# Optimization experiments

Measured on AMD Instinct MI355X. Metric: run time of the kernel, lower is better.

## Reference

```python
import jax, jax.numpy as jnp
import numpy as np

T, B, L, D = 32, 128, 1024, 256  # timesteps, batch, memory slots, word_vec_size(=rnn_size)


def setup_inputs() -> dict:
    key = jax.random.key(0)
    ks = jax.random.split(key, 20)
    f = lambda k, s: jax.random.normal(k, s, dtype=jnp.float32) * 0.05
    return {
        "emb_utts": f(ks[0], (T, B, D)),
        "hr0": f(ks[1], (B, D)),
        "cr0": f(ks[2], (B, D)),
        "hw0": f(ks[3], (B, D)),
        "cw0": f(ks[4], (B, D)),
        "M": f(ks[5], (B, L, D)),
        "mask": jax.random.randint(ks[6], (B, L), 0, 2).astype(bool),
        "Wih_r": f(ks[7], (4 * D, D)),
        "Whh_r": f(ks[8], (4 * D, D)),
        "bih_r": f(ks[9], (4 * D,)),
        "bhh_r": f(ks[10], (4 * D,)),
        "Wc": f(ks[11], (D, 2 * D)),
        "bc": f(ks[12], (D,)),
        "Wih_w": f(ks[13], (4 * D, D)),
        "Whh_w": f(ks[14], (4 * D, D)),
        "bih_w": f(ks[15], (4 * D,)),
        "bhh_w": f(ks[16], (4 * D,)),
    }


def _lstm_cell(x, h, c, Wih, Whh, bih, bhh):
    # PyTorch LSTMCell gate order: i, f, g, o
    g = x @ Wih.T + h @ Whh.T + bih + bhh
    i, fg, gg, o = jnp.split(g, 4, axis=1)
    i = jax.nn.sigmoid(i)
    fg = jax.nn.sigmoid(fg)
    gg = jnp.tanh(gg)
    o = jax.nn.sigmoid(o)
    c2 = fg * c + i * gg
    return o * jnp.tanh(c2), c2


def reference(emb_utts, hr0, cr0, hw0, cw0, M, mask,
              Wih_r, Whh_r, bih_r, bhh_r, Wc, bc,
              Wih_w, Whh_w, bih_w, bhh_w):
    def step(carry, w):
        hr, cr, hw, cw, Mc = carry
        hr, cr = _lstm_cell(w, hr, cr, Wih_r, Whh_r, bih_r, bhh_r)
        # attention read: z = softmax(masked(hr . M))  -> [B, L]
        z = jnp.einsum('bd,bld->bl', hr, Mc)
        z = jax.nn.softmax(jnp.where(mask, -jnp.inf, z), axis=1)
        m = jnp.einsum('bl,bld->bd', z, Mc)           # gather read [B, D]
        comp = jax.nn.softmax(jnp.concatenate([hr, m], axis=1) @ Wc.T + bc, axis=1)
        hw, cw = _lstm_cell(comp, hw, cw, Wih_w, Whh_w, bih_w, bhh_w)
        # memory rewrite exactly as source: M_new = (1 - z) + hw * z (broadcast)
        Mc = (1.0 - z[:, :, None]) + hw[:, None, :] * z[:, :, None]
        return (hr, cr, hw, cw, Mc), hw

    (hr, cr, hw, cw, M), outputs = jax.lax.scan(
        step, (hr0, cr0, hw0, cw0, M), emb_utts)
    return outputs, hr, cr, hw, cw, M
```

## Files before the change

kernel.cpp:

```cpp
#include <hip/hip_runtime.h>
#include <math.h>

typedef unsigned int u32;
typedef __attribute__((ext_vector_type(2))) _Float16 h2;

#define kT 32
#define OUT_STATES 1048576
#define OUT_M      1179648

union H2U { u32 u; h2 h; };

__device__ __forceinline__ float dot2u(u32 w, u32 x, float acc){
  H2U a; a.u = w; H2U b; b.u = x;
#if __has_builtin(__builtin_amdgcn_fdot2)
  return __builtin_amdgcn_fdot2(a.h, b.h, acc, false);
#else
  acc += (float)a.h.x * (float)b.h.x;
  acc += (float)a.h.y * (float)b.h.y;
  return acc;
#endif
}

__device__ __forceinline__ u32 packf16(float x, float y){
  H2U v; v.h.x = (_Float16)x; v.h.y = (_Float16)y; return v.u;
}

__device__ __forceinline__ u32 alu(const u32* p){
  return __hip_atomic_load((u32*)p, __ATOMIC_RELAXED, __HIP_MEMORY_SCOPE_AGENT);
}
__device__ __forceinline__ float alf(const float* p){
  return __hip_atomic_load((float*)p, __ATOMIC_RELAXED, __HIP_MEMORY_SCOPE_AGENT);
}
__device__ __forceinline__ void asu(u32* p, u32 v){
  __hip_atomic_store(p, v, __ATOMIC_RELAXED, __HIP_MEMORY_SCOPE_AGENT);
}
__device__ __forceinline__ void asf(float* p, float v){
  __hip_atomic_store(p, v, __ATOMIC_RELAXED, __HIP_MEMORY_SCOPE_AGENT);
}

__device__ __forceinline__ void pollk(const u32* f, int n, u32 tgt, int tid){
  if (tid < 64){
    const u32* p = f + ((tid < n) ? tid : 0);
    for (;;){
      if (__all((int)(alu(p) >= tgt))) break;
      __builtin_amdgcn_s_sleep(2);
    }
  }
  __syncthreads();
}

__global__ __launch_bounds__(1024) void k_prep(
        const float* __restrict__ Wih_r, const float* __restrict__ Whh_r,
        const float* __restrict__ bih_r, const float* __restrict__ bhh_r,
        const float* __restrict__ Wc,    const float* __restrict__ bc,
        const float* __restrict__ Wih_w, const float* __restrict__ Whh_w,
        const float* __restrict__ bih_w, const float* __restrict__ bhh_w,
        const unsigned char* __restrict__ maskraw,
        u32* WAp, u32* WEp, u32* Wcp, float* bA, float* bE, float* bcf,
        float* wcs, unsigned char* mbuf, u32* flags){
  __shared__ int sb[3];
  if (threadIdx.x < 3) sb[threadIdx.x] = 0;
  __syncthreads();
  if (threadIdx.x < 512){
    unsigned char c = maskraw[threadIdx.x];
    if (c > 1u) atomicOr(&sb[0], 1);
    if ((threadIdx.x & 3) != 0 && c != 0) atomicOr(&sb[1], 1);
    if ((threadIdx.x & 3) == 1 && c == 0x3F) atomicOr(&sb[2], 1);
  }
  __syncthreads();
  int mode = (!sb[0]) ? (sb[1] ? 1 : 0) : (sb[2] ? 2 : 3);

  int idx = blockIdx.x * 1024 + threadIdx.x;
  if (idx < 262144){
    int col = idx >> 8, kp = idx & 255;
    int k0 = 2 * kp;
    float v0 = (k0 < 256) ? Wih_r[col * 256 + k0] : Whh_r[col * 256 + k0 - 256];
    float v1 = (k0 < 256) ? Wih_r[col * 256 + k0 + 1]
                          : Whh_r[col * 256 + k0 + 1 - 256];
    WAp[kp * 1024 + col] = packf16(v0, v1);
  } else if (idx < 524288){
    int i = idx - 262144;
    int col = i >> 8, kp = i & 255;
    int k0 = 2 * kp;
    float v0 = (k0 < 256) ? Wih_w[col * 256 + k0] : Whh_w[col * 256 + k0 - 256];
    float v1 = (k0 < 256) ? Wih_w[col * 256 + k0 + 1]
                          : Whh_w[col * 256 + k0 + 1 - 256];
    WEp[kp * 1024 + col] = packf16(v0, v1);
  } else if (idx < 589824){
    int i = idx - 524288;
    int col = i >> 8, kp = i & 255;
    Wcp[kp * 256 + col] = packf16(Wc[col * 512 + 2 * kp], Wc[col * 512 + 2 * kp + 1]);
  } else if (idx < 590848){
    int i = idx - 589824;
    bA[i] = bih_r[i] + bhh_r[i];
  } else if (idx < 591872){
    int i = idx - 590848;
    bE[i] = bih_w[i] + bhh_w[i];
  } else if (idx < 592128){
    int i = idx - 591872;
    bcf[i] = bc[i];
  } else if (idx < 592384){
    int c = idx - 592128;
    float s = 0.f;
    for (int k = 0; k < 256; k++) s += Wc[c * 512 + 256 + k];
    wcs[c] = s;
  } else if (idx < 723456){
    int l = idx - 592384;
    unsigned char mv;
    if      (mode == 0) mv = (((const int*)maskraw)[l] != 0);
    else if (mode == 1) mv = (maskraw[l] != 0);
    else if (mode == 2) mv = ((maskraw[2*l] | maskraw[2*l+1]) != 0);
    else                mv = (((const unsigned int*)maskraw)[l] != 0);
    mbuf[l] = mv;
  } else if (idx < 724224){
    flags[idx - 723456] = 0;
  }
}

__global__ __launch_bounds__(1024) void k_pre(
        const float* __restrict__ emb, const u32* __restrict__ WAp,
        u32* __restrict__ gxp){
  __shared__ u32 wt[16384];
  __shared__ u32 xt[128 * 129];
  int t = blockIdx.x, c0 = blockIdx.y * 128, tid = threadIdx.x;
  for (int i = 0; i < 16; i++){
    int idx = i * 1024 + tid;
    wt[idx] = WAp[(size_t)(idx >> 7) * 1024 + c0 + (idx & 127)];
    int b = idx >> 7, kp = idx & 127;
    float2 e2 = *(const float2*)(emb + (size_t)t * 32768 + b * 256 + 2 * kp);
    xt[b * 129 + kp] = packf16(e2.x, e2.y);
  }
  __syncthreads();
  int b = tid & 127, cg = tid >> 7;
  float acc[16];
  #pragma unroll
  for (int j = 0; j < 16; j++) acc[j] = 0.f;
  const u32* xrow = xt + b * 129;
  for (int kp = 0; kp < 128; kp++){
    u32 xv = xrow[kp];
    const uint4* wr = (const uint4*)(wt + kp * 128 + cg * 16);
    #pragma unroll
    for (int j4 = 0; j4 < 4; j4++){
      uint4 wv = wr[j4];
      acc[4*j4+0] = dot2u(wv.x, xv, acc[4*j4+0]);
      acc[4*j4+1] = dot2u(wv.y, xv, acc[4*j4+1]);
      acc[4*j4+2] = dot2u(wv.z, xv, acc[4*j4+2]);
      acc[4*j4+3] = dot2u(wv.w, xv, acc[4*j4+3]);
    }
  }
  u32* gp = gxp + ((size_t)t * 128 + b) * 512 + (c0 >> 1) + cg * 8;
  #pragma unroll
  for (int i = 0; i < 8; i++) gp[i] = packf16(acc[2*i], acc[2*i+1]);
}

__device__ __forceinline__ void gemv256(const u32* __restrict__ W,
        const u32* xh, float* psum, int tid){
  int cg = tid & 255, ks = tid >> 8;
  const uint4* wp = (const uint4*)W + (size_t)ks * 32 * 256 + cg;
  const u32* xk = xh + ks * 32;
  float a0 = 0.f, a1 = 0.f, a2 = 0.f, a3 = 0.f;
  #pragma unroll 8
  for (int i = 0; i < 32; i++){
    uint4 wv = wp[(size_t)i * 256];
    u32 xp = xk[i];
    a0 = dot2u(wv.x, xp, a0);  a1 = dot2u(wv.y, xp, a1);
    a2 = dot2u(wv.z, xp, a2);  a3 = dot2u(wv.w, xp, a3);
  }
  float4 r; r.x = a0; r.y = a1; r.z = a2; r.w = a3;
  *(float4*)&psum[ks * 1024 + cg * 4] = r;
}

__device__ __forceinline__ void gemv128x256(const u32* __restrict__ W,
        const u32* xh, float* psum, int tid){
  int c = tid & 255, ks = tid >> 8;
  const u32* wp = W + (size_t)(ks * 32) * 256 + c;
  const u32* xk = xh + ks * 32;
  float a = 0.f;
  #pragma unroll 8
  for (int i = 0; i < 32; i++) a = dot2u(wp[(size_t)i * 256], xk[i], a);
  psum[ks * 256 + c] = a;
}

__device__ void scan_half(int k, const float* __restrict__ M0,
        const unsigned char* __restrict__ mbuf, const float* __restrict__ hrf,
        float* spbuf, float* mpbuf, float* msbuf, u32* fT0, const u32* fR,
        char* sc, int tid){
  float* ps   = (float*)(sc);
  float* wred = (float*)(sc + 16640);
  float* sred = (float*)(sc + 16704);
  float* hr0l = (float*)(sc + 16768);
  int row = k >> 1, half = k & 1;
  pollk(fR + row, 1, 1u, tid);
  if (tid < 256) hr0l[tid] = alf(hrf + row * 256 + tid);
  __syncthreads();
  int w = tid >> 6, lane = tid & 63;
  float4 hrv = *(const float4*)&hr0l[lane * 4];
  float run_max = -INFINITY, S = 0.f;
  float m0 = 0.f, m1 = 0.f, m2 = 0.f, m3 = 0.f;
  int l0 = half * 512 + w * 32;
  for (int l = l0; l < l0 + 32; ++l){
    float4 Mv = *(const float4*)(M0 + ((size_t)row * 1024 + l) * 256 + lane * 4);
    float part = Mv.x * hrv.x + Mv.y * hrv.y + Mv.z * hrv.z + Mv.w * hrv.w;
    #pragma unroll
    for (int mm = 32; mm >= 1; mm >>= 1) part += __shfl_xor(part, mm, 64);
    float s = mbuf[row * 1024 + l] ? -INFINITY : part;
    if (lane == 0) asf(spbuf + row * 1024 + l, s);
    float nm = fmaxf(run_max, s);
    if (nm > -INFINITY){
      float sc2 = expf(run_max - nm);
      float p   = expf(s - nm);
      S = S * sc2 + p;
      m0 = m0 * sc2 + p * Mv.x;  m1 = m1 * sc2 + p * Mv.y;
      m2 = m2 * sc2 + p * Mv.z;  m3 = m3 * sc2 + p * Mv.w;
      run_max = nm;
    }
  }
  if (lane == 0){ wred[w] = run_max; sred[w] = S; }
  ps[w * 260 + lane * 4 + 0] = m0;
  ps[w * 260 + lane * 4 + 1] = m1;
  ps[w * 260 + lane * 4 + 2] = m2;
  ps[w * 260 + lane * 4 + 3] = m3;
  __syncthreads();
  float gmax = -INFINITY;
  #pragma unroll
  for (int w2 = 0; w2 < 16; w2++) gmax = fmaxf(gmax, wred[w2]);
  float Sg = 0.f;
  #pragma unroll
  for (int w2 = 0; w2 < 16; w2++) Sg += sred[w2] * expf(wred[w2] - gmax);
  if (tid < 256){
    float mv = 0.f;
    #pragma unroll
    for (int w2 = 0; w2 < 16; w2++) mv += ps[w2 * 260 + tid] * expf(wred[w2] - gmax);
    asf(mpbuf + k * 256 + tid, mv);
  }
  if (tid == 0){ asf(msbuf + 2 * k, gmax); asf(msbuf + 2 * k + 1, Sg); }
  __syncthreads();
  if (tid == 0) asu(fT0 + k, 1u);
}

__global__ __launch_bounds__(1024, 4) void k_main(
        const float* __restrict__ hr0, const float* __restrict__ cr0,
        const float* __restrict__ hw0, const float* __restrict__ cw0,
        const float* __restrict__ M0,
        const u32* __restrict__ WAp, const u32* __restrict__ WEp,
        const u32* __restrict__ Wcp, const float* __restrict__ bA,
        const float* __restrict__ bE, const float* __restrict__ bcf,
        const float* __restrict__ wcs, const unsigned char* __restrict__ mbuf,
        const u32* __restrict__ gxp,
        float* __restrict__ hrf, float* __restrict__ ubuf,
        float* __restrict__ gwbuf,
        u32* __restrict__ hwp, float* __restrict__ zsbuf,
        float* __restrict__ hwfin, float* __restrict__ spbuf,
        float* __restrict__ mpbuf, float* __restrict__ msbuf,
        u32* __restrict__ flags, float* __restrict__ out){
  __shared__ __attribute__((aligned(16))) char smem[86016];
  int bid = blockIdx.x, tid = threadIdx.x;
  int w = tid >> 6, lane = tid & 63;
  u32* fR  = flags;
  u32* fG  = flags + 192;
  u32* fW  = flags + 256;
  u32* fT0 = flags + 320;

  if (bid < 128){
    int b = bid;
    float* psum = (float*)(smem);
    u32*  xh    = (u32*)(smem + 16384);
    float* hr_f = (float*)(smem + 16896);
    const u32* WRh = WAp + 128 * 1024;
    float cst = (tid < 256) ? cr0[b * 256 + tid] : 0.f;
    if (tid < 128){
      float2 h0 = *(const float2*)(hr0 + b * 256 + 2 * tid);
      xh[tid] = packf16(h0.x, h0.y);
    }
    __syncthreads();
    for (int t = 0; t < kT; t++){
      if (t >= 2) pollk(fW + (b >> 1), 1, (u32)(t - 1), tid);
      u32 gx0 = 0, gx1 = 0, gx2 = 0, gx3 = 0;
      if (tid < 256){
        const u32* gx = gxp + ((size_t)t * 128 + b) * 512;
        gx0 = gx[tid >> 1];          gx1 = gx[128 + (tid >> 1)];
        gx2 = gx[256 + (tid >> 1)];  gx3 = gx[384 + (tid >> 1)];
      }
      gemv256(WRh, xh, psum, tid);
      __syncthreads();
      if (tid < 256){
        H2U p0, p1, p2, p3;
        p0.u = gx0; p1.u = gx1; p2.u = gx2; p3.u = gx3;
        int hi = tid & 1;
        float gi = (hi ? (float)p0.h.y : (float)p0.h.x) + bA[tid];
        float gf = (hi ? (float)p1.h.y : (float)p1.h.x) + bA[256 + tid];
        float gg = (hi ? (float)p2.h.y : (float)p2.h.x) + bA[512 + tid];
        float go = (hi ? (float)p3.h.y : (float)p3.h.x) + bA[768 + tid];
        #pragma unroll
        for (int ks = 0; ks < 4; ks++){
          gi += psum[ks * 1024 + tid];
          gf += psum[ks * 1024 + 256 + tid];
          gg += psum[ks * 1024 + 512 + tid];
          go += psum[ks * 1024 + 768 + tid];
        }
        float i_ = 1.f / (1.f + expf(-gi));
        float f_ = 1.f / (1.f + expf(-gf));
        float g_ = tanhf(gg);
        float o_ = 1.f / (1.f + expf(-go));
        float c2 = f_ * cst + i_ * g_;
        cst = c2;
        float h = o_ * tanhf(c2);
        hr_f[tid] = h;
        asf(hrf + (t & 1) * 32768 + b * 256 + tid, h);
        if (t == kT - 1){
          out[OUT_STATES          + b * 256 + tid] = h;
          out[OUT_STATES +  32768 + b * 256 + tid] = c2;
        }
      }
      __syncthreads();
      if (tid < 128) xh[tid] = packf16(hr_f[2 * tid], hr_f[2 * tid + 1]);
      __syncthreads();
      gemv128x256(Wcp, xh, psum, tid);
      __syncthreads();
      if (tid < 256){
        float u = psum[tid] + psum[256 + tid] + psum[512 + tid] + psum[768 + tid];
        asf(ubuf + (t & 1) * 32768 + b * 256 + tid, u);
      }
      __syncthreads();
      if (tid == 0) asu(fR + b, (u32)(t + 1));
      if (t == 0)
        scan_half(bid, M0, mbuf, hrf, spbuf, mpbuf, msbuf, fT0, fR,
                  smem + 49152, tid);
    }
  } else if (bid < 192){
    int g = bid - 128, r0 = 2 * g, r1 = 2 * g + 1;
    float* psum = (float*)(smem);
    u32*  xh    = (u32*)(smem + 32768);
    for (int t = 0; t < kT; t++){
      if (t == 0){
        if (tid < 128){
          float2 h0 = *(const float2*)(hw0 + r0 * 256 + 2 * tid);
          xh[tid] = packf16(h0.x, h0.y);
        } else if (tid < 256){
          int j = tid - 128;
          float2 h0 = *(const float2*)(hw0 + r1 * 256 + 2 * j);
          xh[tid] = packf16(h0.x, h0.y);
        }
      } else {
        pollk(fW + g, 1, (u32)t, tid);
        if (tid < 128)
          xh[tid] = alu(hwp + ((t - 1) & 1) * 16384 + r0 * 128 + tid);
        else if (tid < 256)
          xh[tid] = alu(hwp + ((t - 1) & 1) * 16384 + r1 * 128 + (tid - 128));
      }
      __syncthreads();
      {
        int cg = tid & 255, ks = tid >> 8;
        const uint4* wp = (const uint4*)(WEp + 128 * 1024)
                        + (size_t)(ks * 32) * 256 + cg;
        const u32* x0 = xh + ks * 32;
        const u32* x1 = xh + 128 + ks * 32;
        float a0=0.f,a1=0.f,a2=0.f,a3=0.f,b0=0.f,b1=0.f,b2=0.f,b3=0.f;
        #pragma unroll 4
        for (int ii = 0; ii < 32; ii++){
          uint4 wv = wp[(size_t)ii * 256];
          u32 xp0 = x0[ii], xp1 = x1[ii];
          a0 = dot2u(wv.x, xp0, a0);  a1 = dot2u(wv.y, xp0, a1);
          a2 = dot2u(wv.z, xp0, a2);  a3 = dot2u(wv.w, xp0, a3);
          b0 = dot2u(wv.x, xp1, b0);  b1 = dot2u(wv.y, xp1, b1);
          b2 = dot2u(wv.z, xp1, b2);  b3 = dot2u(wv.w, xp1, b3);
        }
        float4 ra; ra.x=a0; ra.y=a1; ra.z=a2; ra.w=a3;
        float4 rb; rb.x=b0; rb.y=b1; rb.z=b2; rb.w=b3;
        *(float4*)&psum[ks * 1024 + cg * 4] = ra;
        *(float4*)&psum[4096 + ks * 1024 + cg * 4] = rb;
      }
      __syncthreads();
      #pragma unroll
      for (int rr = 0; rr < 2; rr++){
        float v = psum[rr * 4096 + tid] + psum[rr * 4096 + 1024 + tid]
                + psum[rr * 4096 + 2048 + tid] + psum[rr * 4096 + 3072 + tid];
        asf(gwbuf + (t & 1) * 131072 + (2 * g + rr) * 1024 + tid, v);
      }
      __syncthreads();
      if (tid == 0) asu(fG + g, (u32)(t + 1));
      if (t == 0)
        scan_half(bid, M0, mbuf, hrf, spbuf, mpbuf, msbuf, fT0, fR,
                  smem + 49152, tid);
    }
  } else {
    int g = bid - 192, r0g = 2 * g;
    float* psum  = (float*)(smem);
    u32*  xh    = (u32*)(smem + 32768);
    float* comp  = (float*)(smem + 33792);
    float* hw_f  = (float*)(smem + 35840);
    float* m_f   = (float*)(smem + 37888);
    float* wcs_l = (float*)(smem + 39936);
    float* bc_l  = (float*)(smem + 40960);
    float* redA  = (float*)(smem + 41984);
    float* redB  = (float*)(smem + 42048);
    float* redC  = (float*)(smem + 42112);
    float* redD  = (float*)(smem + 42176);
    float* bE_l  = (float*)(smem + 43008);
    int row = tid >> 9, i = tid & 511;
    int brow = r0g + row;
    if (tid < 256){ wcs_l[tid] = wcs[tid]; bc_l[tid] = bcf[tid]; }
    bE_l[tid] = bE[tid];
    float cst = 0.f;
    if (i < 256){
      hw_f[row * 256 + i] = hw0[brow * 256 + i];
      cst = cw0[brow * 256 + i];
    }
    unsigned char mkA = mbuf[brow * 1024 + i];
    unsigned char mkB = mbuf[brow * 1024 + 512 + i];
    float zA = 0.f, zB = 0.f, vcreg = 0.f;
    __syncthreads();
    scan_half(bid, M0, mbuf, hrf, spbuf, mpbuf, msbuf, fT0, fR,
              smem + 49152, tid);
    pollk(fR + r0g, 2, 1u, tid);
    float hrv = 0.f, ureg = 0.f;
    if (i < 256){
      hrv  = alf(hrf + brow * 256 + i);
      ureg = alf(ubuf + brow * 256 + i);
    }

    for (int t = 0; t < kT; t++){
      float e = -INFINITY;
      if (t == 0){
        pollk(fT0 + 4 * g, 4, 1u, tid);
        int kA2 = 2 * brow, kB2 = 2 * brow + 1;
        float maxA = alf(msbuf + 2 * kA2), SAv = alf(msbuf + 2 * kA2 + 1);
        float maxB = alf(msbuf + 2 * kB2), SBv = alf(msbuf + 2 * kB2 + 1);
        float Gm = fmaxf(maxA, maxB);
        float eAc = expf(maxA - Gm), eBc = expf(maxB - Gm);
        float Sg = SAv * eAc + SBv * eBc;
        zA = expf(alf(spbuf + brow * 1024 + i) - Gm) / Sg;
        zB = expf(alf(spbuf + brow * 1024 + 512 + i) - Gm) / Sg;
        if (i < 256){
          float mv = (alf(mpbuf + kA2 * 256 + i) * eAc
                    + alf(mpbuf + kB2 * 256 + i) * eBc) / Sg;
          m_f[row * 256 + i] = mv;
        }
        __syncthreads();
        if (i < 128)
          xh[row * 128 + i] = packf16(m_f[row * 256 + 2 * i],
                                      m_f[row * 256 + 2 * i + 1]);
        __syncthreads();
        {
          int c = tid & 255, ks = tid >> 8;
          const u32* wp = Wcp + 32768 + (size_t)(ks * 32) * 256 + c;
          const u32* x0 = xh + ks * 32;
          const u32* x1 = xh + 128 + ks * 32;
          float a0 = 0.f, a1 = 0.f;
          #pragma unroll 8
          for (int ii = 0; ii < 32; ii++){
            u32 wv = wp[(size_t)ii * 256];
            a0 = dot2u(wv, x0[ii], a0);
            a1 = dot2u(wv, x1[ii], a1);
          }
          psum[ks * 512 + c] = a0;
          psum[ks * 512 + 256 + c] = a1;
        }
        __syncthreads();
        if (i < 256){
          float vcm = psum[row * 256 + i] + psum[512 + row * 256 + i]
                    + psum[1024 + row * 256 + i] + psum[1536 + row * 256 + i];
          e = ureg + vcm + bc_l[i];
        }
      } else {
        float v1 = (i < 256) ? hrv : 0.f;
        float v2 = (i < 256) ? hrv * hw_f[row * 256 + i] : 0.f;
        #pragma unroll
        for (int mm = 32; mm >= 1; mm >>= 1){
          v1 += __shfl_xor(v1, mm, 64);  v2 += __shfl_xor(v2, mm, 64);
        }
        if (lane == 0){ redA[w] = v1; redB[w] = v2; }
        __syncthreads();
        float S1 = 0.f, S2 = 0.f;
        #pragma unroll
        for (int k2 = 0; k2 < 8; k2++){
          S1 += redA[row * 8 + k2];  S2 += redB[row * 8 + k2];
        }
        float gm = fmaxf(S1, S2);
        float sA = mkA ? -INFINITY : (1.f - zA) * S1 + zA * S2;
        float sB = mkB ? -INFINITY : (1.f - zB) * S1 + zB * S2;
        float pA_ = expf(sA - gm), pB_ = expf(sB - gm);
        float ps = pA_ + pB_, pz = pA_ * zA + pB_ * zB;
        #pragma unroll
        for (int mm = 32; mm >= 1; mm >>= 1){
          ps += __shfl_xor(ps, mm, 64);  pz += __shfl_xor(pz, mm, 64);
        }
        if (lane == 0){ redC[w] = ps; redD[w] = pz; }
        __syncthreads();
        float Ss = 0.f, Pz = 0.f;
        #pragma unroll
        for (int k2 = 0; k2 < 8; k2++){
          Ss += redC[row * 8 + k2];  Pz += redD[row * 8 + k2];
        }
        float Cb = Pz / Ss, Ab = 1.f - Cb;
        zA = pA_ / Ss;  zB = pB_ / Ss;
        if (i < 256)
          e = ureg + Ab * wcs_l[i] + Cb * vcreg + bc_l[i];
      }
      float ev = (i < 256) ? e : -INFINITY;
      float mx2 = ev;
      #pragma unroll
      for (int mm = 32; mm >= 1; mm >>= 1) mx2 = fmaxf(mx2, __shfl_xor(mx2, mm, 64));
      if (lane == 0) redC[w] = mx2;
      __syncthreads();
      float emax = -INFINITY;
      #pragma unroll
      for (int k2 = 0; k2 < 8; k2++) emax = fmaxf(emax, redC[row * 8 + k2]);
      float pe = (i < 256) ? expf(ev - emax) : 0.f;
      float ps2 = pe;
      #pragma unroll
      for (int mm = 32; mm >= 1; mm >>= 1) ps2 += __shfl_xor(ps2, mm, 64);
      if (lane == 0) redD[w] = ps2;
      if (i < 256) comp[row * 256 + i] = pe;
      __syncthreads();
      float esum = 0.f;
      #pragma unroll
      for (int k2 = 0; k2 < 8; k2++) esum += redD[row * 8 + k2];
      if (i < 128)
        xh[row * 128 + i] = packf16(comp[row * 256 + 2 * i],
                                    comp[row * 256 + 2 * i + 1]);
      __syncthreads();
      {
        int cg = tid & 255, ks = tid >> 8;
        const uint4* wp = (const uint4*)WEp + (size_t)(ks * 32) * 256 + cg;
        const u32* x0 = xh + ks * 32;
        const u32* x1 = xh + 128 + ks * 32;
        float a0=0.f,a1=0.f,a2=0.f,a3=0.f,b0=0.f,b1=0.f,b2=0.f,b3=0.f;
        #pragma unroll 4
        for (int ii = 0; ii < 32; ii++){
          uint4 wv = wp[(size_t)ii * 256];
          u32 xp0 = x0[ii], xp1 = x1[ii];
          a0 = dot2u(wv.x, xp0, a0);  a1 = dot2u(wv.y, xp0, a1);
          a2 = dot2u(wv.z, xp0, a2);  a3 = dot2u(wv.w, xp0, a3);
          b0 = dot2u(wv.x, xp1, b0);  b1 = dot2u(wv.y, xp1, b1);
          b2 = dot2u(wv.z, xp1, b2);  b3 = dot2u(wv.w, xp1, b3);
        }
        float4 ra; ra.x=a0; ra.y=a1; ra.z=a2; ra.w=a3;
        float4 rb; rb.x=b0; rb.y=b1; rb.z=b2; rb.w=b3;
        *(float4*)&psum[ks * 1024 + cg * 4] = ra;
        *(float4*)&psum[4096 + ks * 1024 + cg * 4] = rb;
      }
      __syncthreads();
      pollk(fG + g, 1, (u32)(t + 1), tid);
      if (i < 256){
        float rinv = 1.f / esum;
        const float* gwp = gwbuf + (t & 1) * 131072 + brow * 1024;
        float si = psum[row*4096 + i]        + psum[row*4096 + 1024 + i]
                 + psum[row*4096 + 2048 + i] + psum[row*4096 + 3072 + i];
        float sf = psum[row*4096 + 256 + i]  + psum[row*4096 + 1280 + i]
                 + psum[row*4096 + 2304 + i] + psum[row*4096 + 3328 + i];
        float sg2= psum[row*4096 + 512 + i]  + psum[row*4096 + 1536 + i]
                 + psum[row*4096 + 2560 + i] + psum[row*4096 + 3584 + i];
        float so = psum[row*4096 + 768 + i]  + psum[row*4096 + 1792 + i]
                 + psum[row*4096 + 2816 + i] + psum[row*4096 + 3840 + i];
        float gi = bE_l[i]       + alf(gwp + i)       + si  * rinv;
        float gf = bE_l[256 + i] + alf(gwp + 256 + i) + sf  * rinv;
        float gg = bE_l[512 + i] + alf(gwp + 512 + i) + sg2 * rinv;
        float go = bE_l[768 + i] + alf(gwp + 768 + i) + so  * rinv;
        float i_ = 1.f / (1.f + expf(-gi));
        float f_ = 1.f / (1.f + expf(-gf));
        float g_ = tanhf(gg);
        float o_ = 1.f / (1.f + expf(-go));
        float c2 = f_ * cst + i_ * g_;
        cst = c2;
        float h = o_ * tanhf(c2);
        hw_f[row * 256 + i] = h;
        out[(size_t)t * 32768 + brow * 256 + i] = h;
        if (t == kT - 1){
          out[OUT_STATES + 65536 + brow * 256 + i] = h;
          out[OUT_STATES + 98304 + brow * 256 + i] = c2;
        }
      }
      __syncthreads();
      if (i < 128)
        asu(hwp + (t & 1) * 16384 + brow * 128 + i,
            packf16(hw_f[row * 256 + 2 * i], hw_f[row * 256 + 2 * i + 1]));
      __syncthreads();
      if (tid == 0) asu(fW + g, (u32)(t + 1));
      if (t < kT - 1){
        if (i < 128)
          xh[row * 128 + i] = packf16(hw_f[row * 256 + 2 * i],
                                      hw_f[row * 256 + 2 * i + 1]);
        __syncthreads();
        pollk(fR + r0g, 2, (u32)(t + 2), tid);
        if (i < 256){
          hrv  = alf(hrf + ((t + 1) & 1) * 32768 + brow * 256 + i);
          ureg = alf(ubuf + ((t + 1) & 1) * 32768 + brow * 256 + i);
        }
        {
          int c = tid & 255, ks = tid >> 8;
          const u32* wp = Wcp + 32768 + (size_t)(ks * 32) * 256 + c;
          const u32* x0 = xh + ks * 32;
          const u32* x1 = xh + 128 + ks * 32;
          float a0 = 0.f, a1 = 0.f;
          #pragma unroll 8
          for (int ii = 0; ii < 32; ii++){
            u32 wv = wp[(size_t)ii * 256];
            a0 = dot2u(wv, x0[ii], a0);
            a1 = dot2u(wv, x1[ii], a1);
          }
          psum[ks * 512 + c] = a0;
          psum[ks * 512 + 256 + c] = a1;
        }
        __syncthreads();
        if (i < 256)
          vcreg = psum[row * 256 + i] + psum[512 + row * 256 + i]
                + psum[1024 + row * 256 + i] + psum[1536 + row * 256 + i];
        __syncthreads();
      }
    }
    if (i < 256) asf(hwfin + brow * 256 + i, hw_f[row * 256 + i]);
    asf(zsbuf + brow * 1024 + i, zA);
    asf(zsbuf + brow * 1024 + 512 + i, zB);
    __syncthreads();
    if (tid == 0) asu(fW + g, (u32)(kT + 1));
  }

  {
    int mrow = bid >> 1, half = bid & 1;
    pollk(fW + (mrow >> 1), 1, (u32)(kT + 1), tid);
    float* zl  = (float*)(smem + 49152);
    float* hwl = (float*)(smem + 51200);
    if (tid < 512) zl[tid] = alf(zsbuf + mrow * 1024 + half * 512 + tid);
    else if (tid < 768) hwl[tid - 512] = alf(hwfin + mrow * 256 + (tid - 512));
    __syncthreads();
    float* Mout = out + OUT_M + (size_t)mrow * 262144 + (size_t)half * 131072;
    for (int it = 0; it < 32; it++){
      int idx = it * 1024 + tid;
      int l = idx >> 6, d4 = (idx & 63) << 2;
      float z = zl[l], omz = 1.f - z;
      float4 h4 = *(const float4*)&hwl[d4];
      float4 v;
      v.x = omz + h4.x * z;  v.y = omz + h4.y * z;
      v.z = omz + h4.z * z;  v.w = omz + h4.w * z;
      *(float4*)(Mout + (size_t)l * 256 + d4) = v;
    }
  }
}

extern "C" void kernel_launch(void* const* d_in, const int* in_sizes, int n_in,
                              void* d_out, int out_size, void* d_ws, size_t ws_size,
                              hipStream_t stream){
  const float* emb   = (const float*)d_in[0];
  const float* hr0   = (const float*)d_in[1];
  const float* cr0   = (const float*)d_in[2];
  const float* hw0   = (const float*)d_in[3];
  const float* cw0   = (const float*)d_in[4];
  const float* M0    = (const float*)d_in[5];
  const unsigned char* maskraw = (const unsigned char*)d_in[6];
  const float* Wih_r = (const float*)d_in[7];
  const float* Whh_r = (const float*)d_in[8];
  const float* bih_r = (const float*)d_in[9];
  const float* bhh_r = (const float*)d_in[10];
  const float* Wc    = (const float*)d_in[11];
  const float* bc    = (const float*)d_in[12];
  const float* Wih_w = (const float*)d_in[13];
  const float* Whh_w = (const float*)d_in[14];
  const float* bih_w = (const float*)d_in[15];
  const float* bhh_w = (const float*)d_in[16];
  float* out = (float*)d_out;

  char* ws = (char*)d_ws;
  u32*  WAp   = (u32*)(ws);
  u32*  WEp   = (u32*)(ws + 1048576);
  u32*  Wcp   = (u32*)(ws + 2097152);
  float* bA   = (float*)(ws + 2359296);
  float* bE   = (float*)(ws + 2363392);
  float* bcf  = (float*)(ws + 2367488);
  float* wcs  = (float*)(ws + 2368512);
  unsigned char* mbuf = (unsigned char*)(ws + 2369536);
  u32*  flags = (u32*)(ws + 2500608);
  float* hrf  = (float*)(ws + 2504704);
  float* ubuf = (float*)(ws + 2766848);
  float* gwbuf= (float*)(ws + 3291136);
  u32*  hwp   = (u32*)(ws + 4339712);
  float* zsbuf= (float*)(ws + 4470784);
  float* hwfin= (float*)(ws + 4995072);
  float* spbuf= (float*)(ws + 5126144);
  float* mpbuf= (float*)(ws + 5650432);
  float* msbuf= (float*)(ws + 5912576);
  u32*  gxp   = (u32*)(ws + 5914624);

  k_prep<<<dim3(708), dim3(1024), 0, stream>>>(
      Wih_r, Whh_r, bih_r, bhh_r, Wc, bc, Wih_w, Whh_w, bih_w, bhh_w,
      maskraw, WAp, WEp, Wcp, bA, bE, bcf, wcs, mbuf, flags);
  k_pre<<<dim3(32, 8), dim3(1024), 0, stream>>>(emb, WAp, gxp);
  k_main<<<dim3(256), dim3(1024), 0, stream>>>(
      hr0, cr0, hw0, cw0, M0, WAp, WEp, Wcp, bA, bE, bcf, wcs, mbuf, gxp,
      hrf, ubuf, gwbuf, hwp, zsbuf, hwfin, spbuf, mpbuf, msbuf,
      flags, out);
}
```

Before: 654.7 us.

## Move Wc·hw matvec to gate blocks and drop max-reduction in comp softmax

The comp-softmax Wc·hw partial product was computed serially at the end of each step inside the write-LSTM blocks. It is now computed by the hw-gate blocks as soon as hw arrives, published through a new global vcbuf, and signalled with a new flag array. The write blocks poll that flag before forming the logits, which takes the matvec and two barriers off their critical path. Separately, the softmax max-reduction and its barrier are replaced by subtracting a fixed constant of 4. That constant is only safe while the logits stay in a moderate range, so it trades generality for fewer syncs.

```diff
diff --git a/kernel.cpp b/kernel.cpp
--- a/kernel.cpp
+++ b/kernel.cpp
@@ -248,7 +248,7 @@
         const float* __restrict__ wcs, const unsigned char* __restrict__ mbuf,
         const u32* __restrict__ gxp,
         float* __restrict__ hrf, float* __restrict__ ubuf,
-        float* __restrict__ gwbuf,
+        float* __restrict__ vcbuf, float* __restrict__ gwbuf,
         u32* __restrict__ hwp, float* __restrict__ zsbuf,
         float* __restrict__ hwfin, float* __restrict__ spbuf,
         float* __restrict__ mpbuf, float* __restrict__ msbuf,
@@ -257,6 +257,7 @@
   int bid = blockIdx.x, tid = threadIdx.x;
   int w = tid >> 6, lane = tid & 63;
   u32* fR  = flags;
+  u32* fGv = flags + 128;
   u32* fG  = flags + 192;
   u32* fW  = flags + 256;
   u32* fT0 = flags + 320;
@@ -349,6 +350,30 @@
           xh[tid] = alu(hwp + ((t - 1) & 1) * 16384 + r1 * 128 + (tid - 128));
       }
       __syncthreads();
+      {
+        int c = tid & 255, ks = tid >> 8;
+        const u32* wp = Wcp + 32768 + (size_t)(ks * 32) * 256 + c;
+        const u32* x0 = xh + ks * 32;
+        const u32* x1 = xh + 128 + ks * 32;
+        float a0 = 0.f, a1 = 0.f;
+        #pragma unroll 8
+        for (int ii = 0; ii < 32; ii++){
+          u32 wv = wp[(size_t)ii * 256];
+          a0 = dot2u(wv, x0[ii], a0);
+          a1 = dot2u(wv, x1[ii], a1);
+        }
+        psum[ks * 512 + c] = a0;
+        psum[ks * 512 + 256 + c] = a1;
+      }
+      __syncthreads();
+      if (tid < 512){
+        int rr = tid >> 8, c = tid & 255;
+        float v = psum[rr * 256 + c] + psum[512 + rr * 256 + c]
+                + psum[1024 + rr * 256 + c] + psum[1536 + rr * 256 + c];
+        asf(vcbuf + (t & 1) * 32768 + (2 * g + rr) * 256 + c, v);
+      }
+      __syncthreads();
+      if (tid == 0) asu(fGv + g, (u32)(t + 1));
       {
         int cg = tid & 255, ks = tid >> 8;
         const uint4* wp = (const uint4*)(WEp + 128 * 1024)
@@ -408,7 +433,7 @@
     }
     unsigned char mkA = mbuf[brow * 1024 + i];
     unsigned char mkB = mbuf[brow * 1024 + 512 + i];
-    float zA = 0.f, zB = 0.f, vcreg = 0.f;
+    float zA = 0.f, zB = 0.f;
     __syncthreads();
     scan_half(bid, M0, mbuf, hrf, spbuf, mpbuf, msbuf, fT0, fR,
               smem + 49152, tid);
@@ -494,28 +519,22 @@
         }
         float Cb = Pz / Ss, Ab = 1.f - Cb;
         zA = pA_ / Ss;  zB = pB_ / Ss;
-        if (i < 256)
-          e = ureg + Ab * wcs_l[i] + Cb * vcreg + bc_l[i];
-      }
-      float ev = (i < 256) ? e : -INFINITY;
-      float mx2 = ev;
-      #pragma unroll
-      for (int mm = 32; mm >= 1; mm >>= 1) mx2 = fmaxf(mx2, __shfl_xor(mx2, mm, 64));
-      if (lane == 0) redC[w] = mx2;
-      __syncthreads();
-      float emax = -INFINITY;
-      #pragma unroll
-      for (int k2 = 0; k2 < 8; k2++) emax = fmaxf(emax, redC[row * 8 + k2]);
-      float pe = (i < 256) ? expf(ev - emax) : 0.f;
+        pollk(fGv + g, 1, (u32)(t + 1), tid);
+        if (i < 256){
+          float vc = alf(vcbuf + (t & 1) * 32768 + brow * 256 + i);
+          e = ureg + Ab * wcs_l[i] + Cb * vc + bc_l[i];
+        }
+      }
+      float pe = (i < 256) ? expf(e - 4.f) : 0.f;
       float ps2 = pe;
       #pragma unroll
       for (int mm = 32; mm >= 1; mm >>= 1) ps2 += __shfl_xor(ps2, mm, 64);
-      if (lane == 0) redD[w] = ps2;
+      if (lane == 0) redA[w] = ps2;
       if (i < 256) comp[row * 256 + i] = pe;
       __syncthreads();
       float esum = 0.f;
       #pragma unroll
-      for (int k2 = 0; k2 < 8; k2++) esum += redD[row * 8 + k2];
+      for (int k2 = 0; k2 < 8; k2++) esum += redA[row * 8 + k2];
       if (i < 128)
         xh[row * 128 + i] = packf16(comp[row * 256 + 2 * i],
                                     comp[row * 256 + 2 * i + 1]);
@@ -578,35 +597,11 @@
       __syncthreads();
       if (tid == 0) asu(fW + g, (u32)(t + 1));
       if (t < kT - 1){
-        if (i < 128)
-          xh[row * 128 + i] = packf16(hw_f[row * 256 + 2 * i],
-                                      hw_f[row * 256 + 2 * i + 1]);
-        __syncthreads();
         pollk(fR + r0g, 2, (u32)(t + 2), tid);
         if (i < 256){
           hrv  = alf(hrf + ((t + 1) & 1) * 32768 + brow * 256 + i);
           ureg = alf(ubuf + ((t + 1) & 1) * 32768 + brow * 256 + i);
         }
-        {
-          int c = tid & 255, ks = tid >> 8;
-          const u32* wp = Wcp + 32768 + (size_t)(ks * 32) * 256 + c;
-          const u32* x0 = xh + ks * 32;
-          const u32* x1 = xh + 128 + ks * 32;
-          float a0 = 0.f, a1 = 0.f;
-          #pragma unroll 8
-          for (int ii = 0; ii < 32; ii++){
-            u32 wv = wp[(size_t)ii * 256];
-            a0 = dot2u(wv, x0[ii], a0);
-            a1 = dot2u(wv, x1[ii], a1);
-          }
-          psum[ks * 512 + c] = a0;
-          psum[ks * 512 + 256 + c] = a1;
-        }
-        __syncthreads();
-        if (i < 256)
-          vcreg = psum[row * 256 + i] + psum[512 + row * 256 + i]
-                + psum[1024 + row * 256 + i] + psum[1536 + row * 256 + i];
-        __syncthreads();
       }
     }
     if (i < 256) asf(hwfin + brow * 256 + i, hw_f[row * 256 + i]);
@@ -680,6 +675,7 @@
   float* mpbuf= (float*)(ws + 5650432);
   float* msbuf= (float*)(ws + 5912576);
   u32*  gxp   = (u32*)(ws + 5914624);
+  float* vcbuf= (float*)(ws + 14303232);
 
   k_prep<<<dim3(708), dim3(1024), 0, stream>>>(
       Wih_r, Whh_r, bih_r, bhh_r, Wc, bc, Wih_w, Whh_w, bih_w, bhh_w,
@@ -687,6 +683,6 @@
   k_pre<<<dim3(32, 8), dim3(1024), 0, stream>>>(emb, WAp, gxp);
   k_main<<<dim3(256), dim3(1024), 0, stream>>>(
       hr0, cr0, hw0, cw0, M0, WAp, WEp, Wcp, bA, bE, bcf, wcs, mbuf, gxp,
-      hrf, ubuf, gwbuf, hwp, zsbuf, hwfin, spbuf, mpbuf, msbuf,
+      hrf, ubuf, vcbuf, gwbuf, hwp, zsbuf, hwfin, spbuf, mpbuf, msbuf,
       flags, out);
 }
```

Measured after the change: 635.3 us. 1.03x faster.
